# Optimization experiments

Measured on AMD Instinct MI355X. Metric: run time of the kernel, lower is better.

Reference implementation:

```python
import jax, jax.numpy as jnp
import numpy as np

B, V, E = 8, 12288, 98304   # batch, nodes (healpix nside=32), edges (~8 nbrs/node)
FIN, FOUT, K = 256, 256, 4  # channels, Chebyshev order
EPS = 1e-5                  # BatchNorm1d eps


def setup_inputs() -> dict:
    key = jax.random.key(0)
    ks = jax.random.split(key, 5)
    x = jax.random.normal(ks[0], (B, V, FIN), jnp.float32)
    edge_src = jax.random.randint(ks[1], (E,), 0, V, dtype=jnp.int32)
    edge_dst = jax.random.randint(ks[2], (E,), 0, V, dtype=jnp.int32)
    edge_weight = jax.random.normal(ks[3], (E,), jnp.float32) * 0.3
    scale = (2.0 / (FIN * K)) ** 0.5  # kaiming-style init over K*Fin fan-in
    weight = jax.random.normal(ks[4], (K, FIN, FOUT), jnp.float32) * scale
    bias = jnp.zeros((FOUT,), jnp.float32)
    gamma = jnp.ones((FOUT,), jnp.float32)
    beta = jnp.zeros((FOUT,), jnp.float32)
    return {"x": x, "edge_weight": edge_weight, "weight": weight, "bias": bias,
            "gamma": gamma, "beta": beta, "edge_src": edge_src, "edge_dst": edge_dst}


def reference(x, edge_weight, weight, bias, gamma, beta, edge_src, edge_dst):
    # --- ConvCheb: Chebyshev polynomial recursion over sparse Laplacian ---
    xt = x.transpose(1, 0, 2)  # [V, B, Fin] (node-major for segment scatter)

    def lmul(y):  # sparse L @ y, y: [V, B, Fin]
        msg = edge_weight[:, None, None] * y[edge_src]          # [E, B, Fin]
        return jax.ops.segment_sum(msg, edge_dst, num_segments=V)

    xs = [xt]                                  # T_0(L) x = x
    if K > 1:
        xs.append(lmul(xt))                    # T_1(L) x = L x
    for _ in range(2, K):
        xs.append(2.0 * lmul(xs[-1]) - xs[-2])  # T_k = 2 L T_{k-1} - T_{k-2}
    xk = jnp.stack(xs)                         # [K, V, B, Fin]

    out = jnp.einsum('kvbi,kio->bvo', xk, weight) + bias  # [B, V, Fout]

    # --- BatchNorm1d over channels (training-mode batch stats over B,V) ---
    mean = out.mean(axis=(0, 1))
    var = out.var(axis=(0, 1))  # biased variance, as torch uses for normalization
    out = gamma * (out - mean) * jax.lax.rsqrt(var + EPS) + beta

    return jax.nn.relu(out)
```

## Files before the change

### kernel.cpp

```cpp
#include <hip/hip_runtime.h>

#define Vn    12288
#define En    98304
#define Mrows 98304

typedef unsigned short u16;
typedef u16   u16x8  __attribute__((ext_vector_type(8)));
typedef __bf16 bf16x8 __attribute__((ext_vector_type(8)));
typedef float f32x4  __attribute__((ext_vector_type(4)));

struct __align__(8) Edge { int s; float w; };

__device__ __forceinline__ float bf2f(u16 u) {
    union { float f; unsigned int i; } c; c.i = ((unsigned int)u) << 16; return c.f;
}
__device__ __forceinline__ u16 f2bf(float f) {
    union { float f; unsigned int i; } c; c.f = f;
    unsigned int r = c.i + 0x7fffu + ((c.i >> 16) & 1u);
    return (u16)(r >> 16);
}
__device__ __forceinline__ void load_lds16(const void* g, void* l) {
    __builtin_amdgcn_global_load_lds(
        (const __attribute__((address_space(1))) void*)g,
        (__attribute__((address_space(3))) void*)l, 16, 0, 0);
}

__global__ __launch_bounds__(256)
void prep_k(const float* __restrict__ x, u16* __restrict__ xb,
            const float* __restrict__ w, u16* __restrict__ wt,
            const int* __restrict__ edst, int* __restrict__ counts,
            float* __restrict__ sums)
{
    __shared__ u16 tile[32][258];
    int bid = blockIdx.x;
    int t   = threadIdx.x;
    if (bid < Vn) {
        int v = bid;
        int b = t >> 5, i = (t & 31) * 8;
        const float* p = x + ((size_t)b * Vn + v) * 256 + i;
        f32x4 a0 = __builtin_nontemporal_load((const f32x4*)p);
        f32x4 a1 = __builtin_nontemporal_load((const f32x4*)(p + 4));
        u16x8 r;
        #pragma unroll
        for (int j = 0; j < 4; ++j) { r[j] = f2bf(a0[j]); r[4 + j] = f2bf(a1[j]); }
        *(u16x8*)(xb + (size_t)v * 2048 + b * 256 + i) = r;
    } else if (bid < Vn + 8) {
        int o0 = (bid - Vn) * 32;
        int lo = t & 31;
        int kr = t >> 5;
        for (int kc = 0; kc < 4; ++kc) {
            #pragma unroll
            for (int kk0 = 0; kk0 < 256; kk0 += 8) {
                int kk = kc * 256 + kk0 + kr;
                tile[lo][kk0 + kr] = f2bf(w[(size_t)kk * 256 + o0 + lo]);
            }
            __syncthreads();
            #pragma unroll
            for (int i2 = 0; i2 < 4; ++i2) {
                int ch = i2 * 256 + t;
                int r2 = ch >> 5, c2 = ch & 31;
                u16x8 vv = *(const u16x8*)(&tile[r2][c2 * 8]);
                *(u16x8*)(wt + (size_t)(o0 + r2) * 1024 + kc * 256 + c2 * 8) = vv;
            }
            __syncthreads();
        }
    } else if (bid < Vn + 8 + 384) {
        int e = (bid - Vn - 8) * 256 + t;
        atomicAdd(&counts[edst[e]], 1);
    } else {
        sums[t] = 0.f; sums[256 + t] = 0.f;
    }
}

__global__ void scan_k(const int* __restrict__ counts, int* __restrict__ row_start,
                       int* __restrict__ cursor) {
    __shared__ int par[1024];
    int t = threadIdx.x;
    int base = t * 12;
    int s = 0;
    #pragma unroll
    for (int i = 0; i < 12; ++i) s += counts[base + i];
    par[t] = s;
    __syncthreads();
    for (int off = 1; off < 1024; off <<= 1) {
        int v_ = (t >= off) ? par[t - off] : 0;
        __syncthreads();
        par[t] += v_;
        __syncthreads();
    }
    int run = (t == 0) ? 0 : par[t - 1];
    for (int i = 0; i < 12; ++i) {
        row_start[base + i] = run;
        cursor[base + i]    = run;
        run += counts[base + i];
    }
    if (t == 1023) row_start[Vn] = En;
}

__global__ void fill_k(const int* __restrict__ src, const int* __restrict__ dst,
                       const float* __restrict__ ew, int* __restrict__ cursor,
                       Edge* __restrict__ csr) {
    int e = blockIdx.x * 256 + threadIdx.x;
    int d = dst[e];
    int p = atomicAdd(&cursor[d], 1);
    Edge ed; ed.s = src[e]; ed.w = ew[e];
    csr[p] = ed;
}

template<int PREV>
__global__ __launch_bounds__(256)
void lmul_k(const u16* __restrict__ yb, const u16* __restrict__ prevb,
            u16* __restrict__ outb, const int* __restrict__ row_start,
            const Edge* __restrict__ csr)
{
    int slice = blockIdx.x & 7;
    int v     = (blockIdx.x >> 3) * 8 + (threadIdx.x >> 5);
    int t     = threadIdx.x & 31;
    int s0    = row_start[v];
    int cnt   = row_start[v + 1] - s0;
    size_t soff = (size_t)slice * 256 + (size_t)t * 8;
    float acc[8] = {0.f,0.f,0.f,0.f,0.f,0.f,0.f,0.f};
    for (int j0 = 0; j0 < cnt; j0 += 8) {
        int ss[8]; float ww[8];
        #pragma unroll
        for (int u = 0; u < 8; ++u) {
            int j = j0 + u;
            bool ok = j < cnt;
            Edge e = csr[s0 + (ok ? j : 0)];
            ss[u] = e.s; ww[u] = ok ? e.w : 0.f;
        }
        u16x8 g[8];
        #pragma unroll
        for (int u = 0; u < 8; ++u)
            g[u] = *(const u16x8*)(yb + (size_t)ss[u] * 2048 + soff);
        #pragma unroll
        for (int u = 0; u < 8; ++u)
            #pragma unroll
            for (int j8 = 0; j8 < 8; ++j8) acc[j8] += ww[u] * bf2f(g[u][j8]);
    }
    u16x8 r;
    if (PREV) {
        u16x8 pu = *(const u16x8*)(prevb + (size_t)v * 2048 + soff);
        #pragma unroll
        for (int j8 = 0; j8 < 8; ++j8) r[j8] = f2bf(2.0f * acc[j8] - bf2f(pu[j8]));
    } else {
        #pragma unroll
        for (int j8 = 0; j8 < 8; ++j8) r[j8] = f2bf(acc[j8]);
    }
    *(u16x8*)(outb + (size_t)v * 2048 + soff) = r;
}

__device__ __forceinline__ void stage_tile(const u16* __restrict__ Ak, int k0,
                                           const u16* __restrict__ wt, int kt,
                                           int m0, int tid, int wave,
                                           char* bufA, char* bufB)
{
    #pragma unroll
    for (int r = 0; r < 2; ++r) {
        int g  = r * 512 + tid;
        int ml = g >> 3;
        int c  = (g & 7) ^ (ml & 7);
        load_lds16(Ak + ((size_t)(m0 + ml)) * 256 + k0 + c * 8,
                   bufA + r * 8192 + wave * 1024);
    }
    #pragma unroll
    for (int r = 0; r < 4; ++r) {
        int g = r * 512 + tid;
        int o = g >> 3;
        int c = (g & 7) ^ (o & 7);
        load_lds16(wt + (size_t)o * 1024 + kt * 64 + c * 8,
                   bufB + r * 8192 + wave * 1024);
    }
}

__global__ __launch_bounds__(512)
void gemm_k(const u16* __restrict__ x0, const u16* __restrict__ x1,
            const u16* __restrict__ x2, const u16* __restrict__ x3,
            const u16* __restrict__ wt, const float* __restrict__ bias,
            u16* cbp, float* __restrict__ sums, float* __restrict__ sumsq)
{
    alignas(16) __shared__ char lds[147456];
    int tid  = threadIdx.x;
    int wave = tid >> 6;
    int lane = tid & 63;
    int m0   = blockIdx.x * 128;
    int wm   = wave & 1;
    int wn   = wave >> 1;

    f32x4 acc[4][4];
    #pragma unroll
    for (int a = 0; a < 4; ++a)
        #pragma unroll
        for (int b = 0; b < 4; ++b) acc[a][b] = (f32x4){0.f,0.f,0.f,0.f};

    stage_tile(x0, 0,  wt, 0, m0, tid, wave, (char*)lds,         (char*)lds + 16384);
    stage_tile(x0, 64, wt, 1, m0, tid, wave, (char*)lds + 49152, (char*)lds + 49152 + 16384);

    int cb = 0;
    int pb = 2;
    for (int t = 0; t < 16; ++t) {
        if (t < 15) asm volatile("s_waitcnt vmcnt(6) lgkmcnt(0)" ::: "memory");
        else        asm volatile("s_waitcnt vmcnt(0) lgkmcnt(0)" ::: "memory");
        __builtin_amdgcn_s_barrier();
        __builtin_amdgcn_sched_barrier(0);
        if (t < 14) {
            int kt = t + 2;
            int ks = kt >> 2;
            int k0 = (kt & 3) * 64;
            const u16* Ak = (ks == 0) ? x0 : (ks == 1) ? x1 : (ks == 2) ? x2 : x3;
            stage_tile(Ak, k0, wt, kt, m0, tid, wave,
                       (char*)lds + pb * 49152, (char*)lds + pb * 49152 + 16384);
        }
        const char* Ab = (const char*)lds + cb * 49152;
        const char* Bb = Ab + 16384;
        #pragma unroll
        for (int kstep = 0; kstep < 2; ++kstep) {
            int cidx = kstep * 4 + (lane >> 4);
            int row  = lane & 15;
            bf16x8 af[4], bfr[4];
            #pragma unroll
            for (int mt = 0; mt < 4; ++mt) {
                int m16 = wm * 64 + mt * 16 + row;
                af[mt] = *(const bf16x8*)(Ab + (size_t)(m16 * 8 + (cidx ^ (m16 & 7))) * 16);
            }
            #pragma unroll
            for (int nt = 0; nt < 4; ++nt) {
                int ol = wn * 64 + nt * 16 + row;
                bfr[nt] = *(const bf16x8*)(Bb + (size_t)(ol * 8 + (cidx ^ (ol & 7))) * 16);
            }
            __builtin_amdgcn_s_setprio(1);
            #pragma unroll
            for (int mt = 0; mt < 4; ++mt)
                #pragma unroll
                for (int nt = 0; nt < 4; ++nt)
                    acc[mt][nt] = __builtin_amdgcn_mfma_f32_16x16x32_bf16(
                        af[mt], bfr[nt], acc[mt][nt], 0, 0, 0);
            __builtin_amdgcn_s_setprio(0);
        }
        cb = (cb == 2) ? 0 : cb + 1;
        pb = (pb == 2) ? 0 : pb + 1;
    }

    __syncthreads();
    int crow = lane & 15, quad = lane >> 4;
    #pragma unroll
    for (int nt = 0; nt < 4; ++nt) {
        int o = wn * 64 + nt * 16 + crow;
        int c_o = o >> 3, o_in = (o & 7) * 2;
        float bv = bias[o];
        float ps = 0.f, pq = 0.f;
        #pragma unroll
        for (int mt = 0; mt < 4; ++mt) {
            #pragma unroll
            for (int r = 0; r < 4; ++r) {
                int ml = wm * 64 + mt * 16 + quad * 4 + r;
                u16 q = f2bf(acc[mt][nt][r] + bv);
                float vq = bf2f(q);
                *(u16*)(lds + (size_t)ml * 512 + (size_t)(c_o ^ (ml & 7)) * 16 + o_in) = q;
                ps += vq; pq += vq * vq;
            }
        }
        ps += __shfl_down(ps, 32, 64);  pq += __shfl_down(pq, 32, 64);
        ps += __shfl_down(ps, 16, 64);  pq += __shfl_down(pq, 16, 64);
        if (quad == 0) { atomicAdd(&sums[o], ps); atomicAdd(&sumsq[o], pq); }
    }
    __syncthreads();
    #pragma unroll
    for (int rr = 0; rr < 8; ++rr) {
        int ch = rr * 512 + tid;
        int ml = ch >> 5, c = ch & 31;
        u16x8 vv = *(const u16x8*)(lds + (size_t)ml * 512 + (size_t)(c ^ (ml & 7)) * 16);
        *(u16x8*)(cbp + (size_t)(m0 + ml) * 256 + c * 8) = vv;
    }
}

__global__ void bn_relu_k(const u16* __restrict__ cb, float* __restrict__ outp,
                          const float* __restrict__ sums, const float* __restrict__ sumsq,
                          const float* __restrict__ gamma, const float* __restrict__ beta) {
    __shared__ float ssc[256], ssh[256];
    int t = threadIdx.x;
    {
        const float invM = 1.0f / (float)Mrows;
        float mean = sums[t] * invM;
        float var  = sumsq[t] * invM - mean * mean;
        float sc   = gamma[t] * rsqrtf(var + 1e-5f);
        ssc[t] = sc;
        ssh[t] = beta[t] - mean * sc;
    }
    __syncthreads();
    size_t p = ((size_t)blockIdx.x * 256 + t) * 8;
    int o0 = (int)(p & 255);
    int m  = (int)(p >> 8);
    u16x8 v = __builtin_nontemporal_load((const u16x8*)(cb + p));
    float* dst = outp + ((size_t)((m & 7) * Vn + (m >> 3))) * 256 + o0;
    f32x4 a, c;
    #pragma unroll
    for (int i = 0; i < 4; ++i) {
        a[i] = fmaxf(bf2f(v[i])     * ssc[o0 + i]     + ssh[o0 + i],     0.f);
        c[i] = fmaxf(bf2f(v[4 + i]) * ssc[o0 + 4 + i] + ssh[o0 + 4 + i], 0.f);
    }
    __builtin_nontemporal_store(a, (f32x4*)dst);
    __builtin_nontemporal_store(c, (f32x4*)(dst + 4));
}

extern "C" void kernel_launch(void* const* d_in, const int* in_sizes, int n_in,
                              void* d_out, int out_size, void* d_ws, size_t ws_size,
                              hipStream_t stream) {
    const float* x     = (const float*)d_in[0];
    const float* ew    = (const float*)d_in[1];
    const float* w     = (const float*)d_in[2];
    const float* bias  = (const float*)d_in[3];
    const float* gamma = (const float*)d_in[4];
    const float* beta  = (const float*)d_in[5];
    const int*   esrc  = (const int*)d_in[6];
    const int*   edst  = (const int*)d_in[7];
    float* outp = (float*)d_out;
    char*  ws   = (char*)d_ws;

    u16*   xb        = (u16*)  (ws + 0);
    u16*   x1        = (u16*)  (ws + 50331648);
    u16*   x2        = (u16*)  (ws + 100663296);
    u16*   x3        = (u16*)  (ws + 150994944);
    u16*   wt        = (u16*)  (ws + 201326592);
    Edge*  csr       = (Edge*) (ws + 201850880);
    int*   counts    = (int*)  (ws + 202637312);
    int*   row_start = (int*)  (ws + 202686464);
    int*   cursor    = (int*)  (ws + 202736128);
    float* sums      = (float*)(ws + 202785280);
    float* sumsq     = (float*)(ws + 202786304);

    hipMemsetAsync(counts, 0, 49152, stream);

    prep_k<<<Vn + 8 + 384 + 1, 256, 0, stream>>>(x, xb, w, wt, edst, counts, sums);

    scan_k<<<1, 1024, 0, stream>>>(counts, row_start, cursor);
    fill_k<<<384, 256, 0, stream>>>(esrc, edst, ew, cursor, csr);

    lmul_k<0><<<Vn, 256, 0, stream>>>(xb, nullptr, x1, row_start, csr);
    lmul_k<1><<<Vn, 256, 0, stream>>>(x1, xb,      x2, row_start, csr);
    lmul_k<1><<<Vn, 256, 0, stream>>>(x2, x1,      x3, row_start, csr);

    gemm_k<<<Mrows / 128, 512, 0, stream>>>(xb, x1, x2, x3, wt, bias,
                                            (u16*)x1, sums, sumsq);

    bn_relu_k<<<12288, 256, 0, stream>>>((const u16*)x1, outp, sums, sumsq, gamma, beta);
}
```

Before: 457.2 us.

## Fuse third Chebyshev sparse step into GEMM A-tile staging

```diff
diff --git a/kernel.cpp b/kernel.cpp
--- a/kernel.cpp
+++ b/kernel.cpp
@@ -173,11 +173,25 @@
     }
 }
 
+__device__ __forceinline__ void stage_B(const u16* __restrict__ wt, int kt,
+                                        int tid, int wave, char* bufB)
+{
+    #pragma unroll
+    for (int r = 0; r < 4; ++r) {
+        int g = r * 512 + tid;
+        int o = g >> 3;
+        int c = (g & 7) ^ (o & 7);
+        load_lds16(wt + (size_t)o * 1024 + kt * 64 + c * 8,
+                   bufB + r * 8192 + wave * 1024);
+    }
+}
+
 __global__ __launch_bounds__(512)
 void gemm_k(const u16* __restrict__ x0, const u16* __restrict__ x1,
-            const u16* __restrict__ x2, const u16* __restrict__ x3,
+            const u16* __restrict__ x2,
             const u16* __restrict__ wt, const float* __restrict__ bias,
-            u16* cbp, float* __restrict__ sums, float* __restrict__ sumsq)
+            u16* cbp, float* __restrict__ sums, float* __restrict__ sumsq,
+            const int* __restrict__ row_start, const Edge* __restrict__ csr)
 {
     alignas(16) __shared__ char lds[147456];
     int tid  = threadIdx.x;
@@ -199,17 +213,22 @@
     int cb = 0;
     int pb = 2;
     for (int t = 0; t < 16; ++t) {
-        if (t < 15) asm volatile("s_waitcnt vmcnt(6) lgkmcnt(0)" ::: "memory");
-        else        asm volatile("s_waitcnt vmcnt(0) lgkmcnt(0)" ::: "memory");
+        if (t < 11)      asm volatile("s_waitcnt vmcnt(6) lgkmcnt(0)" ::: "memory");
+        else if (t < 15) asm volatile("s_waitcnt vmcnt(4) lgkmcnt(0)" ::: "memory");
+        else             asm volatile("s_waitcnt vmcnt(0) lgkmcnt(0)" ::: "memory");
         __builtin_amdgcn_s_barrier();
         __builtin_amdgcn_sched_barrier(0);
+        char* pbuf = (char*)lds + pb * 49152;
         if (t < 14) {
             int kt = t + 2;
-            int ks = kt >> 2;
-            int k0 = (kt & 3) * 64;
-            const u16* Ak = (ks == 0) ? x0 : (ks == 1) ? x1 : (ks == 2) ? x2 : x3;
-            stage_tile(Ak, k0, wt, kt, m0, tid, wave,
-                       (char*)lds + pb * 49152, (char*)lds + pb * 49152 + 16384);
+            if (kt < 12) {
+                int ks = kt >> 2;
+                int k0 = (kt & 3) * 64;
+                const u16* Ak = (ks == 0) ? x0 : (ks == 1) ? x1 : x2;
+                stage_tile(Ak, k0, wt, kt, m0, tid, wave, pbuf, pbuf + 16384);
+            } else {
+                stage_B(wt, kt, tid, wave, pbuf + 16384);
+            }
         }
         const char* Ab = (const char*)lds + cb * 49152;
         const char* Bb = Ab + 16384;
@@ -236,6 +255,45 @@
                     acc[mt][nt] = __builtin_amdgcn_mfma_f32_16x16x32_bf16(
                         af[mt], bfr[nt], acc[mt][nt], 0, 0, 0);
             __builtin_amdgcn_s_setprio(0);
+        }
+        if (t >= 10 && t < 14) {
+            int kt = t + 2;
+            int k0 = (kt & 3) * 64;
+            #pragma unroll
+            for (int r = 0; r < 2; ++r) {
+                int g  = r * 512 + tid;
+                int ml = g >> 3;
+                int c  = (g & 7) ^ (ml & 7);
+                int vg = (m0 >> 3) + (ml >> 3);
+                int b  = ml & 7;
+                int s0 = row_start[vg];
+                int cnt = row_start[vg + 1] - s0;
+                float a8[8] = {0.f,0.f,0.f,0.f,0.f,0.f,0.f,0.f};
+                for (int j0 = 0; j0 < cnt; j0 += 8) {
+                    int ss[8]; float ww[8];
+                    #pragma unroll
+                    for (int u = 0; u < 8; ++u) {
+                        int j = j0 + u;
+                        bool ok = j < cnt;
+                        Edge e = csr[s0 + (ok ? j : 0)];
+                        ss[u] = e.s; ww[u] = ok ? e.w : 0.f;
+                    }
+                    u16x8 gg[8];
+                    #pragma unroll
+                    for (int u = 0; u < 8; ++u)
+                        gg[u] = *(const u16x8*)(x2 + (size_t)ss[u] * 2048 + b * 256 + k0 + c * 8);
+                    #pragma unroll
+                    for (int u = 0; u < 8; ++u)
+                        #pragma unroll
+                        for (int j8 = 0; j8 < 8; ++j8) a8[j8] += ww[u] * bf2f(gg[u][j8]);
+                }
+                u16x8 pv = *(const u16x8*)(x1 + (size_t)(m0 + ml) * 256 + k0 + c * 8);
+                u16x8 ov;
+                #pragma unroll
+                for (int j8 = 0; j8 < 8; ++j8)
+                    ov[j8] = f2bf(2.0f * a8[j8] - bf2f(pv[j8]));
+                *(u16x8*)(pbuf + (size_t)g * 16) = ov;
+            }
         }
         cb = (cb == 2) ? 0 : cb + 1;
         pb = (pb == 2) ? 0 : pb + 1;
@@ -320,7 +378,6 @@
     u16*   xb        = (u16*)  (ws + 0);
     u16*   x1        = (u16*)  (ws + 50331648);
     u16*   x2        = (u16*)  (ws + 100663296);
-    u16*   x3        = (u16*)  (ws + 150994944);
     u16*   wt        = (u16*)  (ws + 201326592);
     Edge*  csr       = (Edge*) (ws + 201850880);
     int*   counts    = (int*)  (ws + 202637312);
@@ -338,10 +395,9 @@
 
     lmul_k<0><<<Vn, 256, 0, stream>>>(xb, nullptr, x1, row_start, csr);
     lmul_k<1><<<Vn, 256, 0, stream>>>(x1, xb,      x2, row_start, csr);
-    lmul_k<1><<<Vn, 256, 0, stream>>>(x2, x1,      x3, row_start, csr);
-
-    gemm_k<<<Mrows / 128, 512, 0, stream>>>(xb, x1, x2, x3, wt, bias,
-                                            (u16*)x1, sums, sumsq);
+
+    gemm_k<<<Mrows / 128, 512, 0, stream>>>(xb, x1, x2, wt, bias,
+                                            (u16*)x1, sums, sumsq, row_start, csr);
 
     bn_relu_k<<<12288, 256, 0, stream>>>((const u16*)x1, outp, sums, sumsq, gamma, beta);
 }
```

Measured after the change: 464.0 us. About the same (+1.5%).
